# Optimization experiments

Hardware: AMD Instinct MI355X
Metric: run time of the kernel (lower is better)

The kernel has to match this reference:

```python
import jax, jax.numpy as jnp
import numpy as np

GAMMA = 1.0
ALPHA = 0.5
EPS = 1e-8


def setup_inputs() -> dict:
    key = jax.random.key(0)
    k1, k2 = jax.random.split(key)
    x = jax.random.normal(k1, (2048, 32), dtype=jnp.float32)
    y = jax.random.normal(k2, (2048, 32), dtype=jnp.float32)
    return {"x": x, "y": y}


def _normalize(a):
    # torch: mean/std over batch dim, std is unbiased (ddof=1)
    mu = jnp.mean(a, axis=0, keepdims=True)
    sd = jnp.std(a, axis=0, ddof=1, keepdims=True)
    return (a - mu) / (sd + EPS)


def reference(x, y):
    # Classical RBF kernel on normalized inputs
    xn = _normalize(x)
    yn = _normalize(y)
    d = xn[:, None, :] - yn[None, :, :]            # [N, M, D]
    classical = jnp.exp(-GAMMA * jnp.sum(d * d, axis=-1))  # [N, M]

    # Quantum kernel, analytic closed form:
    # RY(t)|0> = [cos(t/2), sin(t/2)]; product state overlap ->
    # |<psi_x|psi_y>|^2 = prod_i cos^2((x_i - y_i)/2)
    qd = (x[:, None, :] - y[None, :, :]) * 0.5     # [N, M, D]
    quantum = jnp.prod(jnp.square(jnp.cos(qd)), axis=-1)    # [N, M]

    return (1.0 - ALPHA) * classical + ALPHA * quantum
```

## Files before the change

### kernel.cpp

```cpp
#include <hip/hip_runtime.h>
#include <math.h>

#define NROWS 2048
#define DDIM 32
#define SBLK 16
#define SROWS (NROWS / SBLK)

__global__ __launch_bounds__(256) void HybridKernel_stats_partial(
    const float* __restrict__ x, const float* __restrict__ y,
    float* __restrict__ part) {
  const int b = blockIdx.x;
  const int a = b >> 4;
  const int blk = b & (SBLK - 1);
  const float* in = a ? y : x;
  const int t = threadIdx.x;
  const int col = t & 31;
  const int rg = t >> 5;
  float s = 0.f, s2 = 0.f;
  const int r0 = blk * SROWS + rg;
#pragma unroll
  for (int i = 0; i < SROWS / 8; ++i) {
    float v = in[(r0 + i * 8) * DDIM + col];
    s += v;
    s2 = fmaf(v, v, s2);
  }
  __shared__ float ss[8][32];
  __shared__ float sq[8][32];
  ss[rg][col] = s;
  sq[rg][col] = s2;
  __syncthreads();
  if (t < 32) {
    float S = 0.f, Q = 0.f;
#pragma unroll
    for (int g = 0; g < 8; ++g) {
      S += ss[g][t];
      Q += sq[g][t];
    }
    part[b * 64 + t] = S;
    part[b * 64 + 32 + t] = Q;
  }
}

__global__ __launch_bounds__(512, 2) void HybridKernel_main(
    const float* __restrict__ x, const float* __restrict__ y,
    const float* __restrict__ part, float* __restrict__ out) {
  __shared__ float4 sD[2][24 * 128];
  __shared__ float sNrm[2][128];
  __shared__ float sMu[2][32];
  __shared__ float sInv[2][32];

  const int t = threadIdx.x;
  const int i0 = blockIdx.y * 128;
  const int j0 = blockIdx.x * 128;

  float4 gx[2], gy[2];
#pragma unroll
  for (int rep = 0; rep < 2; ++rep) {
    const int u = t + 512 * rep;
    const int row = u >> 3;
    const int q = u & 7;
    gx[rep] = *reinterpret_cast<const float4*>(&x[(i0 + row) * DDIM + q * 4]);
    gy[rep] = *reinterpret_cast<const float4*>(&y[(j0 + row) * DDIM + q * 4]);
  }

  if (t < 64) {
    const int a = t >> 5;
    const int c = t & 31;
    float S = 0.f, Q = 0.f;
#pragma unroll
    for (int bb = 0; bb < SBLK; ++bb) {
      S += part[(a * SBLK + bb) * 64 + c];
      Q += part[(a * SBLK + bb) * 64 + 32 + c];
    }
    const float n = (float)NROWS;
    const float mean = S / n;
    const float var = fmaxf((Q - S * mean) / (n - 1.f), 0.f);
    sMu[a][c] = mean;
    sInv[a][c] = 1.f / (sqrtf(var) + 1e-8f);
  }
  __syncthreads();

#pragma unroll
  for (int rep = 0; rep < 2; ++rep) {
    const int u = t + 512 * rep;
    const int row = u >> 3;
    const int q = u & 7;
#pragma unroll
    for (int side = 0; side < 2; ++side) {
      const float4 g = side ? gy[rep] : gx[rep];
      const float sc = side ? 1.0f : 0.5f;
      const float gv[4] = {g.x, g.y, g.z, g.w};
      float xn[4], hc[4], hs[4];
      float nrm = 0.f;
#pragma unroll
      for (int k = 0; k < 4; ++k) {
        const int d = q * 4 + k;
        xn[k] = (gv[k] - sMu[side][d]) * sInv[side][d];
        nrm = fmaf(xn[k], xn[k], nrm);
        float sn, cs;
        __sincosf(gv[k], &sn, &cs);
        hc[k] = sc * cs;
        hs[k] = sc * sn;
      }
      sD[side][(16 + q) * 128 + (row ^ q)] =
          make_float4(xn[0], xn[1], xn[2], xn[3]);
      const int dp0 = 2 * q, dp1 = 2 * q + 1;
      sD[side][dp0 * 128 + (row ^ (dp0 & 7))] =
          make_float4(hc[0], hs[0], hc[1], hs[1]);
      sD[side][dp1 * 128 + (row ^ (dp1 & 7))] =
          make_float4(hc[2], hs[2], hc[3], hs[3]);
      nrm += __shfl_xor(nrm, 1);
      nrm += __shfl_xor(nrm, 2);
      nrm += __shfl_xor(nrm, 4);
      if ((t & 7) == 0) sNrm[side][row] = nrm;
    }
  }
  __syncthreads();

  const int tx = t & 31;
  const int ty = t >> 5;
  const float4* sD0 = &sD[0][0];
  const float4* sD1 = &sD[1][0];

  float acc[8][4];
  float qp[8][4];
#pragma unroll
  for (int r = 0; r < 8; ++r)
#pragma unroll
    for (int c = 0; c < 4; ++c) {
      acc[r][c] = 0.f;
      qp[r][c] = 1.f;
    }

#pragma unroll
  for (int q = 0; q < 8; ++q) {
    {
      const int S = 16 + q;
      const int sw = S & 7;
      float4 FX[8], FY[4];
#pragma unroll
      for (int i = 0; i < 8; ++i) FX[i] = sD0[S * 128 + ((ty + 16 * i) ^ sw)];
#pragma unroll
      for (int j = 0; j < 4; ++j) FY[j] = sD1[S * 128 + ((tx + 32 * j) ^ sw)];
#pragma unroll
      for (int r = 0; r < 8; ++r)
#pragma unroll
        for (int c = 0; c < 4; ++c) {
          float a = acc[r][c];
          a = fmaf(FX[r].x, FY[c].x, a);
          a = fmaf(FX[r].y, FY[c].y, a);
          a = fmaf(FX[r].z, FY[c].z, a);
          a = fmaf(FX[r].w, FY[c].w, a);
          acc[r][c] = a;
        }
    }
#pragma unroll
    for (int h = 0; h < 2; ++h) {
      const int S = 2 * q + h;
      const int sw = S & 7;
      float4 FX[8], FY[4];
#pragma unroll
      for (int i = 0; i < 8; ++i) FX[i] = sD0[S * 128 + ((ty + 16 * i) ^ sw)];
#pragma unroll
      for (int j = 0; j < 4; ++j) FY[j] = sD1[S * 128 + ((tx + 32 * j) ^ sw)];
#pragma unroll
      for (int r = 0; r < 8; ++r)
#pragma unroll
        for (int c = 0; c < 4; ++c) {
          const float t0 =
              fmaf(FX[r].x, FY[c].x, fmaf(FX[r].y, FY[c].y, 0.5f));
          const float t1 =
              fmaf(FX[r].z, FY[c].z, fmaf(FX[r].w, FY[c].w, 0.5f));
          qp[r][c] *= t0 * t1;
        }
    }
  }

  float nx[8], ny[4];
#pragma unroll
  for (int r = 0; r < 8; ++r) nx[r] = sNrm[0][ty + 16 * r];
#pragma unroll
  for (int c = 0; c < 4; ++c) ny[c] = sNrm[1][tx + 32 * c];

#pragma unroll
  for (int r = 0; r < 8; ++r) {
    const int row = i0 + ty + 16 * r;
    float* o = out + (size_t)row * NROWS + j0;
#pragma unroll
    for (int c = 0; c < 4; ++c) {
      const float cl = __expf(2.f * acc[r][c] - nx[r] - ny[c]);
      o[tx + 32 * c] = 0.5f * (cl + qp[r][c]);
    }
  }
}

extern "C" void kernel_launch(void* const* d_in, const int* in_sizes, int n_in,
                              void* d_out, int out_size, void* d_ws,
                              size_t ws_size, hipStream_t stream) {
  const float* x = (const float*)d_in[0];
  const float* y = (const float*)d_in[1];
  float* part = (float*)d_ws;
  float* out = (float*)d_out;

  HybridKernel_stats_partial<<<2 * SBLK, 256, 0, stream>>>(x, y, part);
  dim3 grid(NROWS / 128, NROWS / 128);
  HybridKernel_main<<<grid, 512, 0, stream>>>(x, y, part, out);
}
```

Baseline: 26.62 us.

## Widen stats partial grid, parallelize stats reduction, restructure main inner loop

The stats pre-pass now runs 32 blocks per input instead of 16, and each thread issues its eight loads up front before accumulating. In the main kernel, all 512 threads reduce the partial sums with 8-lane shuffles, where previously 64 threads each summed serially. The q loop is now kept rolled, with all three slices' shared-memory fragments loaded at the start of each iteration. This is meant to cut serial latency in the prologue and lower register pressure, but the rolled loop gives the compiler less room to schedule across iterations.

```diff
diff --git a/kernel.cpp b/kernel.cpp
--- a/kernel.cpp
+++ b/kernel.cpp
@@ -3,26 +3,28 @@
 
 #define NROWS 2048
 #define DDIM 32
-#define SBLK 16
+#define SBLK 32
 #define SROWS (NROWS / SBLK)
 
 __global__ __launch_bounds__(256) void HybridKernel_stats_partial(
     const float* __restrict__ x, const float* __restrict__ y,
     float* __restrict__ part) {
   const int b = blockIdx.x;
-  const int a = b >> 4;
+  const int a = b >> 5;
   const int blk = b & (SBLK - 1);
   const float* in = a ? y : x;
   const int t = threadIdx.x;
   const int col = t & 31;
   const int rg = t >> 5;
+  const int r0 = blk * SROWS + rg;
+  float v[8];
+#pragma unroll
+  for (int k = 0; k < 8; ++k) v[k] = in[(r0 + 8 * k) * DDIM + col];
   float s = 0.f, s2 = 0.f;
-  const int r0 = blk * SROWS + rg;
-#pragma unroll
-  for (int i = 0; i < SROWS / 8; ++i) {
-    float v = in[(r0 + i * 8) * DDIM + col];
-    s += v;
-    s2 = fmaf(v, v, s2);
+#pragma unroll
+  for (int k = 0; k < 8; ++k) {
+    s += v[k];
+    s2 = fmaf(v[k], v[k], s2);
   }
   __shared__ float ss[8][32];
   __shared__ float sq[8][32];
@@ -63,20 +65,30 @@
     gy[rep] = *reinterpret_cast<const float4*>(&y[(j0 + row) * DDIM + q * 4]);
   }
 
-  if (t < 64) {
-    const int a = t >> 5;
-    const int c = t & 31;
+  {
+    const int a = t >> 8;
+    const int col = (t >> 3) & 31;
+    const int g = t & 7;
     float S = 0.f, Q = 0.f;
 #pragma unroll
-    for (int bb = 0; bb < SBLK; ++bb) {
-      S += part[(a * SBLK + bb) * 64 + c];
-      Q += part[(a * SBLK + bb) * 64 + 32 + c];
-    }
-    const float n = (float)NROWS;
-    const float mean = S / n;
-    const float var = fmaxf((Q - S * mean) / (n - 1.f), 0.f);
-    sMu[a][c] = mean;
-    sInv[a][c] = 1.f / (sqrtf(var) + 1e-8f);
+    for (int m = 0; m < 4; ++m) {
+      const int bb = a * SBLK + g * 4 + m;
+      S += part[bb * 64 + col];
+      Q += part[bb * 64 + 32 + col];
+    }
+    S += __shfl_xor(S, 1);
+    S += __shfl_xor(S, 2);
+    S += __shfl_xor(S, 4);
+    Q += __shfl_xor(Q, 1);
+    Q += __shfl_xor(Q, 2);
+    Q += __shfl_xor(Q, 4);
+    if (g == 0) {
+      const float n = (float)NROWS;
+      const float mean = S / n;
+      const float var = fmaxf((Q - S * mean) / (n - 1.f), 0.f);
+      sMu[a][col] = mean;
+      sInv[a][col] = 1.f / (sqrtf(var) + 1e-8f);
+    }
   }
   __syncthreads();
 
@@ -132,48 +144,60 @@
       qp[r][c] = 1.f;
     }
 
-#pragma unroll
+#pragma unroll 1
   for (int q = 0; q < 8; ++q) {
-    {
-      const int S = 16 + q;
-      const int sw = S & 7;
-      float4 FX[8], FY[4];
-#pragma unroll
-      for (int i = 0; i < 8; ++i) FX[i] = sD0[S * 128 + ((ty + 16 * i) ^ sw)];
-#pragma unroll
-      for (int j = 0; j < 4; ++j) FY[j] = sD1[S * 128 + ((tx + 32 * j) ^ sw)];
-#pragma unroll
-      for (int r = 0; r < 8; ++r)
-#pragma unroll
-        for (int c = 0; c < 4; ++c) {
-          float a = acc[r][c];
-          a = fmaf(FX[r].x, FY[c].x, a);
-          a = fmaf(FX[r].y, FY[c].y, a);
-          a = fmaf(FX[r].z, FY[c].z, a);
-          a = fmaf(FX[r].w, FY[c].w, a);
-          acc[r][c] = a;
-        }
-    }
-#pragma unroll
-    for (int h = 0; h < 2; ++h) {
-      const int S = 2 * q + h;
-      const int sw = S & 7;
-      float4 FX[8], FY[4];
-#pragma unroll
-      for (int i = 0; i < 8; ++i) FX[i] = sD0[S * 128 + ((ty + 16 * i) ^ sw)];
-#pragma unroll
-      for (int j = 0; j < 4; ++j) FY[j] = sD1[S * 128 + ((tx + 32 * j) ^ sw)];
-#pragma unroll
-      for (int r = 0; r < 8; ++r)
-#pragma unroll
-        for (int c = 0; c < 4; ++c) {
-          const float t0 =
-              fmaf(FX[r].x, FY[c].x, fmaf(FX[r].y, FY[c].y, 0.5f));
-          const float t1 =
-              fmaf(FX[r].z, FY[c].z, fmaf(FX[r].w, FY[c].w, 0.5f));
-          qp[r][c] *= t0 * t1;
-        }
-    }
+    const int sC = (16 + q) * 128;
+    const int s0 = (2 * q) * 128;
+    const int s1 = (2 * q + 1) * 128;
+    const int swC = q;
+    const int sw0 = (2 * q) & 7;
+    const int sw1 = (2 * q + 1) & 7;
+
+    float4 FXC[8], FYC[4], FX0[8], FY0[4], FX1[8], FY1[4];
+#pragma unroll
+    for (int i = 0; i < 8; ++i) FXC[i] = sD0[sC + ((ty + 16 * i) ^ swC)];
+#pragma unroll
+    for (int j = 0; j < 4; ++j) FYC[j] = sD1[sC + ((tx + 32 * j) ^ swC)];
+#pragma unroll
+    for (int i = 0; i < 8; ++i) FX0[i] = sD0[s0 + ((ty + 16 * i) ^ sw0)];
+#pragma unroll
+    for (int j = 0; j < 4; ++j) FY0[j] = sD1[s0 + ((tx + 32 * j) ^ sw0)];
+#pragma unroll
+    for (int i = 0; i < 8; ++i) FX1[i] = sD0[s1 + ((ty + 16 * i) ^ sw1)];
+#pragma unroll
+    for (int j = 0; j < 4; ++j) FY1[j] = sD1[s1 + ((tx + 32 * j) ^ sw1)];
+
+#pragma unroll
+    for (int r = 0; r < 8; ++r)
+#pragma unroll
+      for (int c = 0; c < 4; ++c) {
+        float a = acc[r][c];
+        a = fmaf(FXC[r].x, FYC[c].x, a);
+        a = fmaf(FXC[r].y, FYC[c].y, a);
+        a = fmaf(FXC[r].z, FYC[c].z, a);
+        a = fmaf(FXC[r].w, FYC[c].w, a);
+        acc[r][c] = a;
+      }
+#pragma unroll
+    for (int r = 0; r < 8; ++r)
+#pragma unroll
+      for (int c = 0; c < 4; ++c) {
+        const float t0 =
+            fmaf(FX0[r].x, FY0[c].x, fmaf(FX0[r].y, FY0[c].y, 0.5f));
+        const float t1 =
+            fmaf(FX0[r].z, FY0[c].z, fmaf(FX0[r].w, FY0[c].w, 0.5f));
+        qp[r][c] *= t0 * t1;
+      }
+#pragma unroll
+    for (int r = 0; r < 8; ++r)
+#pragma unroll
+      for (int c = 0; c < 4; ++c) {
+        const float t0 =
+            fmaf(FX1[r].x, FY1[c].x, fmaf(FX1[r].y, FY1[c].y, 0.5f));
+        const float t1 =
+            fmaf(FX1[r].z, FY1[c].z, fmaf(FX1[r].w, FY1[c].w, 0.5f));
+        qp[r][c] *= t0 * t1;
+      }
   }
 
   float nx[8], ny[4];
```

Measured after the change: 29.73 us. +11.7%, slower.

## Fuse column-stats pass into main kernel via cooperative grid sync

Applied to the files above, without the earlier changes.

Merges the separate statistics kernel into the main tile kernel. Each of the 256 blocks computes partial sums over 8 rows of x and y, writes them to workspace, and performs a cooperative grid-wide sync. Every block then reduces all 256 partials to get the mean and inverse std. This removes one kernel launch and its gap. In exchange it adds a grid barrier, requires all 256 blocks to be co-resident, and has every block read the full partial array.

```diff
diff --git a/kernel.cpp b/kernel.cpp
--- a/kernel.cpp
+++ b/kernel.cpp
@@ -1,57 +1,26 @@
 #include <hip/hip_runtime.h>
+#include <hip/hip_cooperative_groups.h>
 #include <math.h>
+
+namespace cg = cooperative_groups;
 
 #define NROWS 2048
 #define DDIM 32
-#define SBLK 16
-#define SROWS (NROWS / SBLK)
-
-__global__ __launch_bounds__(256) void HybridKernel_stats_partial(
+
+__global__ __launch_bounds__(512, 2) void HybridKernel_coop(
     const float* __restrict__ x, const float* __restrict__ y,
-    float* __restrict__ part) {
-  const int b = blockIdx.x;
-  const int a = b >> 4;
-  const int blk = b & (SBLK - 1);
-  const float* in = a ? y : x;
-  const int t = threadIdx.x;
-  const int col = t & 31;
-  const int rg = t >> 5;
-  float s = 0.f, s2 = 0.f;
-  const int r0 = blk * SROWS + rg;
-#pragma unroll
-  for (int i = 0; i < SROWS / 8; ++i) {
-    float v = in[(r0 + i * 8) * DDIM + col];
-    s += v;
-    s2 = fmaf(v, v, s2);
-  }
-  __shared__ float ss[8][32];
-  __shared__ float sq[8][32];
-  ss[rg][col] = s;
-  sq[rg][col] = s2;
-  __syncthreads();
-  if (t < 32) {
-    float S = 0.f, Q = 0.f;
-#pragma unroll
-    for (int g = 0; g < 8; ++g) {
-      S += ss[g][t];
-      Q += sq[g][t];
-    }
-    part[b * 64 + t] = S;
-    part[b * 64 + 32 + t] = Q;
-  }
-}
-
-__global__ __launch_bounds__(512, 2) void HybridKernel_main(
-    const float* __restrict__ x, const float* __restrict__ y,
-    const float* __restrict__ part, float* __restrict__ out) {
+    float* __restrict__ part, float* __restrict__ out) {
   __shared__ float4 sD[2][24 * 128];
   __shared__ float sNrm[2][128];
   __shared__ float sMu[2][32];
   __shared__ float sInv[2][32];
+  __shared__ float2 sP[8][32];
 
   const int t = threadIdx.x;
-  const int i0 = blockIdx.y * 128;
-  const int j0 = blockIdx.x * 128;
+  const int bx = blockIdx.x, by = blockIdx.y;
+  const int b = by * 16 + bx;
+  const int i0 = by * 128;
+  const int j0 = bx * 128;
 
   float4 gx[2], gy[2];
 #pragma unroll
@@ -63,20 +32,57 @@
     gy[rep] = *reinterpret_cast<const float4*>(&y[(j0 + row) * DDIM + q * 4]);
   }
 
+  {
+    const int a = t >> 8;
+    const int c = t & 31;
+    const float* in = a ? y : x;
+    const float v = in[(b * 8 + ((t >> 5) & 7)) * DDIM + c];
+    float s = v, s2 = v * v;
+    s += __shfl_xor(s, 32);
+    s2 += __shfl_xor(s2, 32);
+    const int w = t >> 6;
+    if ((t & 63) < 32) sP[w][c] = make_float2(s, s2);
+  }
+  __syncthreads();
   if (t < 64) {
     const int a = t >> 5;
     const int c = t & 31;
     float S = 0.f, Q = 0.f;
 #pragma unroll
-    for (int bb = 0; bb < SBLK; ++bb) {
-      S += part[(a * SBLK + bb) * 64 + c];
-      Q += part[(a * SBLK + bb) * 64 + 32 + c];
-    }
-    const float n = (float)NROWS;
-    const float mean = S / n;
-    const float var = fmaxf((Q - S * mean) / (n - 1.f), 0.f);
-    sMu[a][c] = mean;
-    sInv[a][c] = 1.f / (sqrtf(var) + 1e-8f);
+    for (int w = 0; w < 4; ++w) {
+      S += sP[a * 4 + w][c].x;
+      Q += sP[a * 4 + w][c].y;
+    }
+    part[b * 128 + a * 32 + c] = S;
+    part[b * 128 + 64 + a * 32 + c] = Q;
+  }
+
+  cg::this_grid().sync();
+
+  {
+    const int a = t >> 8;
+    const int c = (t >> 3) & 31;
+    const int g = t & 7;
+    float S = 0.f, Q = 0.f;
+#pragma unroll 8
+    for (int m = 0; m < 32; ++m) {
+      const int bb = g + 8 * m;
+      S += part[bb * 128 + a * 32 + c];
+      Q += part[bb * 128 + 64 + a * 32 + c];
+    }
+    S += __shfl_xor(S, 1);
+    S += __shfl_xor(S, 2);
+    S += __shfl_xor(S, 4);
+    Q += __shfl_xor(Q, 1);
+    Q += __shfl_xor(Q, 2);
+    Q += __shfl_xor(Q, 4);
+    if (g == 0) {
+      const float n = (float)NROWS;
+      const float mean = S / n;
+      const float var = fmaxf((Q - S * mean) / (n - 1.f), 0.f);
+      sMu[a][c] = mean;
+      sInv[a][c] = 1.f / (sqrtf(var) + 1e-8f);
+    }
   }
   __syncthreads();
 
@@ -202,7 +208,7 @@
   float* part = (float*)d_ws;
   float* out = (float*)d_out;
 
-  HybridKernel_stats_partial<<<2 * SBLK, 256, 0, stream>>>(x, y, part);
-  dim3 grid(NROWS / 128, NROWS / 128);
-  HybridKernel_main<<<grid, 512, 0, stream>>>(x, y, part, out);
+  void* args[] = {(void*)&x, (void*)&y, (void*)&part, (void*)&out};
+  hipLaunchCooperativeKernel((const void*)HybridKernel_coop, dim3(16, 16),
+                             dim3(512), args, 0, stream);
 }
```

Result: slower. 62.85 us (+136.1%).

## Compute classical RBF dot products with split-bf16 MFMA instead of FP32 FMAs

Applied to the files above, without the earlier changes.

Moves the 32-dim normalized dot product for the RBF term from scalar FP32 FMAs onto bf16 MFMA 16x16x32 instructions. Each input is split into high and low bf16 parts and three MFMAs are summed to keep near-FP32 accuracy. The thread-to-output mapping changes to match the MFMA accumulator layout, and the quantum cosine product stays on FMAs using the new indices. This frees VALU cycles for the quantum product, at the cost of extra LDS packing and a different output store pattern that may coalesce less well.

```diff
diff --git a/kernel.cpp b/kernel.cpp
--- a/kernel.cpp
+++ b/kernel.cpp
@@ -5,6 +5,9 @@
 #define DDIM 32
 #define SBLK 16
 #define SROWS (NROWS / SBLK)
+
+typedef __attribute__((ext_vector_type(8))) short short8;
+typedef __attribute__((ext_vector_type(4))) float f32x4;
 
 __global__ __launch_bounds__(256) void HybridKernel_stats_partial(
     const float* __restrict__ x, const float* __restrict__ y,
@@ -41,10 +44,15 @@
   }
 }
 
+__device__ __forceinline__ unsigned packbf(float a, float b) {
+  return (__float_as_uint(a) >> 16) | (__float_as_uint(b) & 0xffff0000u);
+}
+
 __global__ __launch_bounds__(512, 2) void HybridKernel_main(
     const float* __restrict__ x, const float* __restrict__ y,
     const float* __restrict__ part, float* __restrict__ out) {
-  __shared__ float4 sD[2][24 * 128];
+  __shared__ float4 sCS[2][16 * 128];
+  __shared__ uint4 sXB[2][2][128 * 5];
   __shared__ float sNrm[2][128];
   __shared__ float sMu[2][32];
   __shared__ float sInv[2][32];
@@ -102,13 +110,23 @@
         hc[k] = sc * cs;
         hs[k] = sc * sn;
       }
-      sD[side][(16 + q) * 128 + (row ^ q)] =
-          make_float4(xn[0], xn[1], xn[2], xn[3]);
       const int dp0 = 2 * q, dp1 = 2 * q + 1;
-      sD[side][dp0 * 128 + (row ^ (dp0 & 7))] =
+      sCS[side][dp0 * 128 + (row ^ (dp0 & 7))] =
           make_float4(hc[0], hs[0], hc[1], hs[1]);
-      sD[side][dp1 * 128 + (row ^ (dp1 & 7))] =
+      sCS[side][dp1 * 128 + (row ^ (dp1 & 7))] =
           make_float4(hc[2], hs[2], hc[3], hs[3]);
+      float hif[4], lof[4];
+#pragma unroll
+      for (int k = 0; k < 4; ++k) {
+        hif[k] = __uint_as_float(__float_as_uint(xn[k]) & 0xffff0000u);
+        lof[k] = xn[k] - hif[k];
+      }
+      char* bh = (char*)&sXB[side][0][0] + row * 80 + q * 8;
+      char* bl = (char*)&sXB[side][1][0] + row * 80 + q * 8;
+      *reinterpret_cast<uint2*>(bh) =
+          make_uint2(packbf(hif[0], hif[1]), packbf(hif[2], hif[3]));
+      *reinterpret_cast<uint2*>(bl) =
+          make_uint2(packbf(lof[0], lof[1]), packbf(lof[2], lof[3]));
       nrm += __shfl_xor(nrm, 1);
       nrm += __shfl_xor(nrm, 2);
       nrm += __shfl_xor(nrm, 4);
@@ -117,79 +135,102 @@
   }
   __syncthreads();
 
-  const int tx = t & 31;
-  const int ty = t >> 5;
-  const float4* sD0 = &sD[0][0];
-  const float4* sD1 = &sD[1][0];
-
-  float acc[8][4];
+  const int w = t >> 6;
+  const int l = t & 63;
+  const int l4 = l >> 4;
+  const int ln = l & 15;
+  const int R0 = (w >> 1) * 32;
+  const int C0 = (w & 1) * 64;
+
+  short8 Ah[2], Al[2], Bh[4], Bl[4];
+  {
+    const char* bxh = (const char*)&sXB[0][0][0];
+    const char* bxl = (const char*)&sXB[0][1][0];
+    const char* byh = (const char*)&sXB[1][0][0];
+    const char* byl = (const char*)&sXB[1][1][0];
+#pragma unroll
+    for (int tr = 0; tr < 2; ++tr) {
+      const int off = (R0 + 16 * tr + ln) * 80 + l4 * 16;
+      Ah[tr] = *reinterpret_cast<const short8*>(bxh + off);
+      Al[tr] = *reinterpret_cast<const short8*>(bxl + off);
+    }
+#pragma unroll
+    for (int tc = 0; tc < 4; ++tc) {
+      const int off = (C0 + 16 * tc + ln) * 80 + l4 * 16;
+      Bh[tc] = *reinterpret_cast<const short8*>(byh + off);
+      Bl[tc] = *reinterpret_cast<const short8*>(byl + off);
+    }
+  }
+  f32x4 dotacc[2][4];
+#pragma unroll
+  for (int tr = 0; tr < 2; ++tr)
+#pragma unroll
+    for (int tc = 0; tc < 4; ++tc) {
+      f32x4 a = {0.f, 0.f, 0.f, 0.f};
+      a = __builtin_amdgcn_mfma_f32_16x16x32_bf16(Ah[tr], Bl[tc], a, 0, 0, 0);
+      a = __builtin_amdgcn_mfma_f32_16x16x32_bf16(Al[tr], Bh[tc], a, 0, 0, 0);
+      a = __builtin_amdgcn_mfma_f32_16x16x32_bf16(Ah[tr], Bh[tc], a, 0, 0, 0);
+      dotacc[tr][tc] = a;
+    }
+
+  int r_idx[8], c_idx[4];
+#pragma unroll
+  for (int ri = 0; ri < 8; ++ri)
+    r_idx[ri] = R0 + 16 * (ri >> 2) + 4 * l4 + (ri & 3);
+#pragma unroll
+  for (int tc = 0; tc < 4; ++tc) c_idx[tc] = C0 + 16 * tc + ln;
+
+  float cl[8][4];
+#pragma unroll
+  for (int tr = 0; tr < 2; ++tr) {
+#pragma unroll
+    for (int mm = 0; mm < 4; ++mm) {
+      const float nx = sNrm[0][r_idx[tr * 4 + mm]];
+#pragma unroll
+      for (int tc = 0; tc < 4; ++tc) {
+        const float ny = sNrm[1][c_idx[tc]];
+        cl[tr * 4 + mm][tc] =
+            __expf(2.f * dotacc[tr][tc][mm] - nx - ny);
+      }
+    }
+  }
+
+  const float4* sCS0 = &sCS[0][0];
+  const float4* sCS1 = &sCS[1][0];
   float qp[8][4];
 #pragma unroll
-  for (int r = 0; r < 8; ++r)
-#pragma unroll
-    for (int c = 0; c < 4; ++c) {
-      acc[r][c] = 0.f;
-      qp[r][c] = 1.f;
-    }
-
-#pragma unroll
-  for (int q = 0; q < 8; ++q) {
-    {
-      const int S = 16 + q;
-      const int sw = S & 7;
-      float4 FX[8], FY[4];
-#pragma unroll
-      for (int i = 0; i < 8; ++i) FX[i] = sD0[S * 128 + ((ty + 16 * i) ^ sw)];
-#pragma unroll
-      for (int j = 0; j < 4; ++j) FY[j] = sD1[S * 128 + ((tx + 32 * j) ^ sw)];
-#pragma unroll
-      for (int r = 0; r < 8; ++r)
-#pragma unroll
-        for (int c = 0; c < 4; ++c) {
-          float a = acc[r][c];
-          a = fmaf(FX[r].x, FY[c].x, a);
-          a = fmaf(FX[r].y, FY[c].y, a);
-          a = fmaf(FX[r].z, FY[c].z, a);
-          a = fmaf(FX[r].w, FY[c].w, a);
-          acc[r][c] = a;
-        }
-    }
-#pragma unroll
-    for (int h = 0; h < 2; ++h) {
-      const int S = 2 * q + h;
-      const int sw = S & 7;
-      float4 FX[8], FY[4];
-#pragma unroll
-      for (int i = 0; i < 8; ++i) FX[i] = sD0[S * 128 + ((ty + 16 * i) ^ sw)];
-#pragma unroll
-      for (int j = 0; j < 4; ++j) FY[j] = sD1[S * 128 + ((tx + 32 * j) ^ sw)];
-#pragma unroll
-      for (int r = 0; r < 8; ++r)
-#pragma unroll
-        for (int c = 0; c < 4; ++c) {
-          const float t0 =
-              fmaf(FX[r].x, FY[c].x, fmaf(FX[r].y, FY[c].y, 0.5f));
-          const float t1 =
-              fmaf(FX[r].z, FY[c].z, fmaf(FX[r].w, FY[c].w, 0.5f));
-          qp[r][c] *= t0 * t1;
-        }
-    }
-  }
-
-  float nx[8], ny[4];
-#pragma unroll
-  for (int r = 0; r < 8; ++r) nx[r] = sNrm[0][ty + 16 * r];
-#pragma unroll
-  for (int c = 0; c < 4; ++c) ny[c] = sNrm[1][tx + 32 * c];
-
-#pragma unroll
-  for (int r = 0; r < 8; ++r) {
-    const int row = i0 + ty + 16 * r;
-    float* o = out + (size_t)row * NROWS + j0;
-#pragma unroll
-    for (int c = 0; c < 4; ++c) {
-      const float cl = __expf(2.f * acc[r][c] - nx[r] - ny[c]);
-      o[tx + 32 * c] = 0.5f * (cl + qp[r][c]);
+  for (int ri = 0; ri < 8; ++ri)
+#pragma unroll
+    for (int tc = 0; tc < 4; ++tc) qp[ri][tc] = 1.f;
+
+#pragma unroll
+  for (int dp = 0; dp < 16; ++dp) {
+    const int sw = dp & 7;
+    float4 FX[8], FY[4];
+#pragma unroll
+    for (int ri = 0; ri < 8; ++ri)
+      FX[ri] = sCS0[dp * 128 + (r_idx[ri] ^ sw)];
+#pragma unroll
+    for (int tc = 0; tc < 4; ++tc)
+      FY[tc] = sCS1[dp * 128 + (c_idx[tc] ^ sw)];
+#pragma unroll
+    for (int ri = 0; ri < 8; ++ri)
+#pragma unroll
+      for (int tc = 0; tc < 4; ++tc) {
+        const float t0 =
+            fmaf(FX[ri].x, FY[tc].x, fmaf(FX[ri].y, FY[tc].y, 0.5f));
+        const float t1 =
+            fmaf(FX[ri].z, FY[tc].z, fmaf(FX[ri].w, FY[tc].w, 0.5f));
+        qp[ri][tc] *= t0 * t1;
+      }
+  }
+
+#pragma unroll
+  for (int ri = 0; ri < 8; ++ri) {
+    float* o = out + (size_t)(i0 + r_idx[ri]) * NROWS + j0;
+#pragma unroll
+    for (int tc = 0; tc < 4; ++tc) {
+      o[c_idx[tc]] = 0.5f * (cl[ri][tc] + qp[ri][tc]);
     }
   }
 }
```

Measured after the change: 24.55 us. 1.08x faster.
